# Optimization experiments

Hardware: AMD Instinct MI355X
Metric: run time of the kernel (lower is better)

The kernel has to match this reference:

```python
import jax, jax.numpy as jnp
import numpy as np

B, N, D, H = 4, 2048, 256, 8
d = D // H          # 32 per-head dim
EPS = 1e-5
SCALE = 1.0 / float(np.sqrt(d))


def setup_inputs() -> dict:
    key = jax.random.key(0)
    ks = jax.random.split(key, 6)
    s = 0.02
    x = jax.random.normal(ks[0], (B, N, D), jnp.float32)
    # RoPE frequencies: theta_j = 10000^(-2j/d), angle = pos * theta
    inv_freq = 1.0 / (10000.0 ** (jnp.arange(0, d, 2, dtype=jnp.float32) / d))  # (d/2,)
    ang = jnp.arange(N, dtype=jnp.float32)[:, None] * inv_freq[None, :]          # (N, d/2)
    return {
        "x": x,
        "freqs_cos": jnp.cos(ang),
        "freqs_sin": jnp.sin(ang),
        "w_qkv": jax.random.normal(ks[1], (D, 3 * D), jnp.float32) * s,
        "b_qkv": jnp.zeros((3 * D,), jnp.float32),
        "w_proj": jax.random.normal(ks[2], (D, D), jnp.float32) * s,
        "b_proj": jnp.zeros((D,), jnp.float32),
        "ln1_g": jnp.ones((D,), jnp.float32),
        "ln1_b": jnp.zeros((D,), jnp.float32),
        "ln2_g": jnp.ones((D,), jnp.float32),
        "ln2_b": jnp.zeros((D,), jnp.float32),
        "w1": jax.random.normal(ks[3], (D, 2 * D), jnp.float32) * s,
        "b1": jnp.zeros((2 * D,), jnp.float32),
        "w2": jax.random.normal(ks[4], (2 * D, D), jnp.float32) * s,
        "b2": jnp.zeros((D,), jnp.float32),
    }


def _layer_norm(x, g, b):
    mu = jnp.mean(x, axis=-1, keepdims=True)
    var = jnp.mean(jnp.square(x - mu), axis=-1, keepdims=True)
    return (x - mu) * jax.lax.rsqrt(var + EPS) * g + b


def _rope(t, cos, sin):
    # t: (B,H,N,d); interleaved (even,odd) pairs viewed as complex, multiplied by e^{i*ang}
    tr = t.reshape(B, H, N, d // 2, 2)
    te, to = tr[..., 0], tr[..., 1]
    c = cos[None, None, :, :]
    s = sin[None, None, :, :]
    oe = te * c - to * s
    oo = te * s + to * c
    return jnp.stack([oe, oo], axis=-1).reshape(B, H, N, d)


def reference(x, freqs_cos, freqs_sin, w_qkv, b_qkv, w_proj, b_proj,
              ln1_g, ln1_b, ln2_g, ln2_b, w1, b1, w2, b2):
    # Pre-LN MHSA with RoPE (dropout = identity at eval)
    h = _layer_norm(x, ln1_g, ln1_b)
    qkv = (h @ w_qkv + b_qkv).reshape(B, N, 3, H, d).transpose(0, 2, 3, 1, 4)  # (B,3,H,N,d)
    q, k, v = qkv[:, 0], qkv[:, 1], qkv[:, 2]
    q = _rope(q, freqs_cos, freqs_sin)
    k = _rope(k, freqs_cos, freqs_sin)
    attn = jax.nn.softmax(jnp.einsum('bhnd,bhmd->bhnm', q, k) * SCALE, axis=-1)
    out = jnp.einsum('bhnm,bhmd->bhnd', attn, v).transpose(0, 2, 1, 3).reshape(B, N, D)
    x = x + (out @ w_proj + b_proj)
    h = _layer_norm(x, ln2_g, ln2_b)
    ffn = jax.nn.relu(h @ w1 + b1) @ w2 + b2
    return x + ffn
```

## Files before the change

kernel.cpp:

```cpp
#include <hip/hip_runtime.h>
#include <hip/hip_bf16.h>
#include <math.h>

#define Bsz 4
#define Nseq 2048
#define Dm 256
#define Hh 8
#define Hd 32
#define EPS_ 1e-5f
#define SCALE_ 0.17677669529663687f
#define QSC_ (0.17677669529663687f * 1.4426950408889634f)

typedef __attribute__((ext_vector_type(8))) short short8;
typedef __attribute__((ext_vector_type(4))) short short4v;
typedef __attribute__((ext_vector_type(4))) float f32x4;
typedef __attribute__((ext_vector_type(16))) float f32x16;

__device__ __forceinline__ void gload16(const void* g, void* l) {
    __builtin_amdgcn_global_load_lds(
        (const __attribute__((address_space(1))) void*)g,
        (__attribute__((address_space(3))) void*)l, 16, 0, 0);
}

__device__ __forceinline__ short bf16s(float f) {
    __hip_bfloat16 h = __float2bfloat16(f);
    return *(short*)&h;
}

union FU { float f; unsigned u; };

__device__ __forceinline__ int pk2bf(float a, float b) {
    FU ua, ub; ua.f = a; ub.f = b;
    return (int)__builtin_amdgcn_perm(ub.u, ua.u, 0x07060302u);
}

union I4S8 { int i[4]; short8 s; };

__global__ __launch_bounds__(256) void prep_kernel(
    const float* __restrict__ x, const float* __restrict__ g1,
    const float* __restrict__ b1v, __hip_bfloat16* __restrict__ hout,
    const float* __restrict__ s0, const float* __restrict__ s1,
    const float* __restrict__ s2, const float* __restrict__ s3,
    __hip_bfloat16* __restrict__ d0, __hip_bfloat16* __restrict__ d1,
    __hip_bfloat16* __restrict__ d2, __hip_bfloat16* __restrict__ d3) {
    __shared__ float t[32][33];
    if (blockIdx.x < 2048) {
        int row  = blockIdx.x * 4 + (threadIdx.x >> 6);
        int lane = threadIdx.x & 63;
        const float* xr = x + (size_t)row * Dm;
        float4 v = *(const float4*)(xr + lane * 4);
        float s  = v.x + v.y + v.z + v.w;
        float ss = v.x * v.x + v.y * v.y + v.z * v.z + v.w * v.w;
        #pragma unroll
        for (int off = 32; off; off >>= 1) {
            s  += __shfl_xor(s, off);
            ss += __shfl_xor(ss, off);
        }
        float mu  = s * (1.0f / Dm);
        float var = ss * (1.0f / Dm) - mu * mu;
        float rs  = rsqrtf(var + EPS_);
        float4 gv = *(const float4*)(g1 + lane * 4);
        float4 bv = *(const float4*)(b1v + lane * 4);
        short4v o4 = { bf16s((v.x - mu) * rs * gv.x + bv.x),
                       bf16s((v.y - mu) * rs * gv.y + bv.y),
                       bf16s((v.z - mu) * rs * gv.z + bv.z),
                       bf16s((v.w - mu) * rs * gv.w + bv.w) };
        *(short4v*)(hout + (size_t)row * Dm + lane * 4) = o4;
        return;
    }
    int bid = blockIdx.x - 2048;
    const float* src; __hip_bfloat16* dst; int K, N, tb;
    if (bid < 192)      { src = s0; dst = d0; K = 256; N = 768; tb = bid; }
    else if (bid < 256) { src = s1; dst = d1; K = 256; N = 256; tb = bid - 192; }
    else if (bid < 384) { src = s2; dst = d2; K = 256; N = 512; tb = bid - 256; }
    else                { src = s3; dst = d3; K = 512; N = 256; tb = bid - 384; }
    int tn = N >> 5;
    int k0 = (tb / tn) * 32, n0 = (tb % tn) * 32;
    int c = threadIdx.x & 31, r0 = threadIdx.x >> 5;
    #pragma unroll
    for (int i = 0; i < 4; i++) {
        int r = r0 + i * 8;
        t[r][c] = src[(size_t)(k0 + r) * N + n0 + c];
    }
    __syncthreads();
    #pragma unroll
    for (int i = 0; i < 4; i++) {
        int n = r0 + i * 8;
        dst[(size_t)(n0 + n) * K + k0 + c] = __float2bfloat16(t[c][n]);
    }
}

__global__ __launch_bounds__(256) void ln_kernel(const float* __restrict__ x,
                                                 const float* __restrict__ g,
                                                 const float* __restrict__ b,
                                                 __hip_bfloat16* __restrict__ out) {
    int row  = blockIdx.x * 4 + (threadIdx.x >> 6);
    int lane = threadIdx.x & 63;
    const float* xr = x + (size_t)row * Dm;
    float4 v = *(const float4*)(xr + lane * 4);
    float s  = v.x + v.y + v.z + v.w;
    float ss = v.x * v.x + v.y * v.y + v.z * v.z + v.w * v.w;
    #pragma unroll
    for (int off = 32; off; off >>= 1) {
        s  += __shfl_xor(s, off);
        ss += __shfl_xor(ss, off);
    }
    float mu  = s * (1.0f / Dm);
    float var = ss * (1.0f / Dm) - mu * mu;
    float rs  = rsqrtf(var + EPS_);
    float4 gv = *(const float4*)(g + lane * 4);
    float4 bv = *(const float4*)(b + lane * 4);
    short4v o4 = { bf16s((v.x - mu) * rs * gv.x + bv.x),
                   bf16s((v.y - mu) * rs * gv.y + bv.y),
                   bf16s((v.z - mu) * rs * gv.z + bv.z),
                   bf16s((v.w - mu) * rs * gv.w + bv.w) };
    *(short4v*)(out + (size_t)row * Dm + lane * 4) = o4;
}

template <int EPI>
__global__ __launch_bounds__(256) void mfma_gemm(const __hip_bfloat16* __restrict__ A,
                                                 const __hip_bfloat16* __restrict__ Wt,
                                                 const float* __restrict__ bias,
                                                 const float* __restrict__ res,
                                                 float* __restrict__ Cf,
                                                 __hip_bfloat16* __restrict__ Cb,
                                                 int M, int Nn, int K) {
    __shared__ __align__(16) __hip_bfloat16 As[2][64 * 64];
    __shared__ __align__(16) __hip_bfloat16 Bs[2][64 * 64];
    const int tid = threadIdx.x, w = tid >> 6, lane = tid & 63;
    const int lm = lane & 15, lq = lane >> 4;
    const int bm = blockIdx.y * 64, bn = blockIdx.x * 64;
    f32x4 acc[4];
    #pragma unroll
    for (int j = 0; j < 4; j++) acc[j] = (f32x4){0.f, 0.f, 0.f, 0.f};

    const int sr = tid >> 3, ssl = tid & 7;
    const int sgk = (ssl ^ (sr & 7)) * 8;
    const int sr2 = 32 + sr;
    const int sgk2 = (ssl ^ (sr2 & 7)) * 8;

    gload16(A + (size_t)(bm + sr) * K + sgk, &As[0][w * 512]);
    gload16(A + (size_t)(bm + sr2) * K + sgk2, &As[0][2048 + w * 512]);
    gload16(Wt + (size_t)(bn + sr) * K + sgk, &Bs[0][w * 512]);
    gload16(Wt + (size_t)(bn + sr2) * K + sgk2, &Bs[0][2048 + w * 512]);

    const int arow = w * 16 + lm;
    const int ar7 = arow & 7, cr7base = lm & 7;
    for (int t = 0; t < K / 64; t++) {
        const int buf = t & 1;
        __syncthreads();
        if (t + 1 < K / 64) {
            int k0 = (t + 1) * 64;
            gload16(A + (size_t)(bm + sr) * K + k0 + sgk, &As[buf ^ 1][w * 512]);
            gload16(A + (size_t)(bm + sr2) * K + k0 + sgk2, &As[buf ^ 1][2048 + w * 512]);
            gload16(Wt + (size_t)(bn + sr) * K + k0 + sgk, &Bs[buf ^ 1][w * 512]);
            gload16(Wt + (size_t)(bn + sr2) * K + k0 + sgk2, &Bs[buf ^ 1][2048 + w * 512]);
        }
        #pragma unroll
        for (int ks = 0; ks < 2; ks++) {
            short8 a = *(const short8*)&As[buf][arow * 64 + (((ks * 4 + lq) ^ ar7) * 8)];
            #pragma unroll
            for (int nf = 0; nf < 4; nf++) {
                int cc = nf * 16 + lm;
                short8 bfr = *(const short8*)&Bs[buf][cc * 64 + (((ks * 4 + lq) ^ (cc & 7)) * 8)];
                acc[nf] = __builtin_amdgcn_mfma_f32_16x16x32_bf16(a, bfr, acc[nf], 0, 0, 0);
            }
        }
    }
    #pragma unroll
    for (int nf = 0; nf < 4; nf++) {
        int cg = bn + nf * 16 + lm;
        float bi = bias[cg];
        #pragma unroll
        for (int r = 0; r < 4; r++) {
            int rg = bm + w * 16 + lq * 4 + r;
            float v = acc[nf][r] + bi;
            if (EPI == 1) {
                v = fmaxf(v, 0.f);
                Cb[(size_t)rg * Nn + cg] = __float2bfloat16(v);
            } else {
                v += res[(size_t)rg * Nn + cg];
                Cf[(size_t)rg * Nn + cg] = v;
            }
        }
    }
}

__global__ __launch_bounds__(256) void qkv_mfma(const __hip_bfloat16* __restrict__ A,
                                                const __hip_bfloat16* __restrict__ Wt,
                                                const float* __restrict__ bias,
                                                const float* __restrict__ fcos,
                                                const float* __restrict__ fsin,
                                                __hip_bfloat16* __restrict__ qout,
                                                __hip_bfloat16* __restrict__ kout,
                                                __hip_bfloat16* __restrict__ vt) {
    const int K = 256;
    __shared__ __align__(16) __hip_bfloat16 As[2][64 * 64];
    __shared__ __align__(16) __hip_bfloat16 Bs[2][64 * 64];
    const int tid = threadIdx.x, w = tid >> 6, lane = tid & 63;
    const int lm = lane & 15, lq = lane >> 4;
    const int bm = blockIdx.y * 64, bn = blockIdx.x * 64;
    f32x4 acc[4];
    #pragma unroll
    for (int j = 0; j < 4; j++) acc[j] = (f32x4){0.f, 0.f, 0.f, 0.f};

    const int sr = tid >> 3, ssl = tid & 7;
    const int sgk = (ssl ^ (sr & 7)) * 8;
    const int sr2 = 32 + sr;
    const int sgk2 = (ssl ^ (sr2 & 7)) * 8;

    gload16(A + (size_t)(bm + sr) * K + sgk, &As[0][w * 512]);
    gload16(A + (size_t)(bm + sr2) * K + sgk2, &As[0][2048 + w * 512]);
    gload16(Wt + (size_t)(bn + sr) * K + sgk, &Bs[0][w * 512]);
    gload16(Wt + (size_t)(bn + sr2) * K + sgk2, &Bs[0][2048 + w * 512]);

    const int arow = w * 16 + lm;
    const int ar7 = arow & 7;
    for (int t = 0; t < K / 64; t++) {
        const int buf = t & 1;
        __syncthreads();
        if (t + 1 < K / 64) {
            int k0 = (t + 1) * 64;
            gload16(A + (size_t)(bm + sr) * K + k0 + sgk, &As[buf ^ 1][w * 512]);
            gload16(A + (size_t)(bm + sr2) * K + k0 + sgk2, &As[buf ^ 1][2048 + w * 512]);
            gload16(Wt + (size_t)(bn + sr) * K + k0 + sgk, &Bs[buf ^ 1][w * 512]);
            gload16(Wt + (size_t)(bn + sr2) * K + k0 + sgk2, &Bs[buf ^ 1][2048 + w * 512]);
        }
        #pragma unroll
        for (int ks = 0; ks < 2; ks++) {
            short8 a = *(const short8*)&As[buf][arow * 64 + (((ks * 4 + lq) ^ ar7) * 8)];
            #pragma unroll
            for (int nf = 0; nf < 4; nf++) {
                int cc = nf * 16 + lm;
                short8 bfr = *(const short8*)&Bs[buf][cc * 64 + (((ks * 4 + lq) ^ (cc & 7)) * 8)];
                acc[nf] = __builtin_amdgcn_mfma_f32_16x16x32_bf16(a, bfr, acc[nf], 0, 0, 0);
            }
        }
    }
    const int seg = bn >> 8;
    #pragma unroll
    for (int nf = 0; nf < 4; nf++) {
        int cg = bn + nf * 16 + lm;
        int hh = (cg & 255) >> 5;
        int dd = (nf & 1) * 16 + lm;
        int i0 = dd >> 1;
        float bi = bias[cg];
        #pragma unroll
        for (int r = 0; r < 4; r++) {
            int rg = bm + w * 16 + lq * 4 + r;
            int bb = rg >> 11, n = rg & (Nseq - 1);
            float v = acc[nf][r] + bi;
            if (seg == 2) {
                vt[(((size_t)(bb * Hh + hh)) * Hd + dd) * Nseq + n] = __float2bfloat16(v);
            } else {
                float vp = __shfl_xor(v, 1);
                float cs = fcos[n * 16 + i0], sn = fsin[n * 16 + i0];
                float outv = (dd & 1) ? (vp * sn + v * cs) : (v * cs - vp * sn);
                if (seg == 0) outv *= QSC_;
                __hip_bfloat16* dst = (seg == 0) ? qout : kout;
                dst[(((size_t)(bb * Hh + hh)) * Nseq + n) * Hd + dd] = __float2bfloat16(outv);
            }
        }
    }
}

__global__ __launch_bounds__(256) void attn_mfma(const __hip_bfloat16* __restrict__ q,
                                                 const __hip_bfloat16* __restrict__ k,
                                                 const __hip_bfloat16* __restrict__ vt,
                                                 __hip_bfloat16* __restrict__ att) {
    __shared__ __align__(16) char smem[4096 + 16384 + 16384 + 512];
    __hip_bfloat16* Qs  = (__hip_bfloat16*)smem;
    __hip_bfloat16* KsB = (__hip_bfloat16*)(smem + 4096);
    __hip_bfloat16* VsB = (__hip_bfloat16*)(smem + 20480);
    float* RedO = (float*)(smem + 4096);
    float* RedS = (float*)(smem + 4096 + 8192);
    float* smS  = (float*)(smem + 4096 + 8192 + 256);

    const int tid = threadIdx.x, w = tid >> 6, lane = tid & 63;
    const int l31 = lane & 31, hi = lane >> 5;
    const int wq = w >> 1, wk = w & 1;
    const int bh = blockIdx.y, qbase = blockIdx.x * 64;
    const __hip_bfloat16* qp = q + ((size_t)bh * Nseq + qbase) * Hd;
    const __hip_bfloat16* kp = k + (size_t)bh * Nseq * Hd;
    const __hip_bfloat16* vp = vt + (size_t)bh * Hd * Nseq;
    const int r8 = tid >> 3, s8 = tid & 7;

    {
        int r = tid >> 2, sl = tid & 3;
        gload16(qp + r * 32 + ((sl ^ (r & 3)) * 8), Qs + w * 512);
    }
    #pragma unroll
    for (int par = 0; par < 2; par++) {
        gload16(kp + (par * 64 + 2 * r8 + (s8 >> 2)) * 32 + (((s8 & 3) ^ (r8 & 3)) * 8),
                KsB + par * 2048 + w * 512);
        gload16(vp + (size_t)r8 * Nseq + par * 64 + ((s8 ^ (r8 & 7)) * 8),
                VsB + par * 2048 + w * 512);
    }
    __syncthreads();

    const int qrow = wq * 32 + l31;
    short8 qf0 = *(const short8*)&Qs[qrow * 32 + ((hi ^ (l31 & 3)) * 8)];
    short8 qf1 = *(const short8*)&Qs[qrow * 32 + (((2 + hi) ^ (l31 & 3)) * 8)];

    f32x16 O;
    #pragma unroll
    for (int i = 0; i < 16; i++) O[i] = 0.f;
    float sm = 0.f;

    for (int t = 0; t < 16; t++) {
        const int buf = t & 1;
        if (t + 1 < 16) {
            const int kb2 = (t + 1) * 128;
            #pragma unroll
            for (int par = 0; par < 2; par++) {
                gload16(kp + (kb2 + par * 64 + 2 * r8 + (s8 >> 2)) * 32 + (((s8 & 3) ^ (r8 & 3)) * 8),
                        KsB + ((buf ^ 1) * 2 + par) * 2048 + w * 512);
                gload16(vp + (size_t)r8 * Nseq + kb2 + par * 64 + ((s8 ^ (r8 & 7)) * 8),
                        VsB + ((buf ^ 1) * 2 + par) * 2048 + w * 512);
            }
        }
        const __hip_bfloat16* Kc = KsB + (buf * 2 + wk) * 2048;
        const __hip_bfloat16* Vc = VsB + (buf * 2 + wk) * 2048;
        f32x16 St0, St1;
        #pragma unroll
        for (int i = 0; i < 16; i++) { St0[i] = 0.f; St1[i] = 0.f; }
        {
            int pr = l31 >> 1, elb = pr * 64 + (l31 & 1) * 32;
            short8 kf0 = *(const short8*)&Kc[elb + ((hi ^ (pr & 3)) * 8)];
            short8 kf1 = *(const short8*)&Kc[elb + (((2 + hi) ^ (pr & 3)) * 8)];
            St0 = __builtin_amdgcn_mfma_f32_32x32x16_bf16(kf0, qf0, St0, 0, 0, 0);
            St0 = __builtin_amdgcn_mfma_f32_32x32x16_bf16(kf1, qf1, St0, 0, 0, 0);
        }
        {
            int pr = 16 + (l31 >> 1), elb = pr * 64 + (l31 & 1) * 32;
            short8 kf0 = *(const short8*)&Kc[elb + ((hi ^ (pr & 3)) * 8)];
            short8 kf1 = *(const short8*)&Kc[elb + (((2 + hi) ^ (pr & 3)) * 8)];
            St1 = __builtin_amdgcn_mfma_f32_32x32x16_bf16(kf0, qf0, St1, 0, 0, 0);
            St1 = __builtin_amdgcn_mfma_f32_32x32x16_bf16(kf1, qf1, St1, 0, 0, 0);
        }
        int pk0[8], pk1[8];
        #pragma unroll
        for (int p = 0; p < 8; p++) {
            float a = __builtin_amdgcn_exp2f(St0[2 * p]);
            float b = __builtin_amdgcn_exp2f(St0[2 * p + 1]);
            sm += a + b;
            pk0[p] = pk2bf(a, b);
        }
        #pragma unroll
        for (int p = 0; p < 8; p++) {
            float a = __builtin_amdgcn_exp2f(St1[2 * p]);
            float b = __builtin_amdgcn_exp2f(St1[2 * p + 1]);
            sm += a + b;
            pk1[p] = pk2bf(a, b);
        }
        #pragma unroll
        for (int tt = 0; tt < 4; tt++) {
            const int* PK = (tt >> 1) ? pk1 : pk0;
            const int base = 4 * (tt & 1);
            int keep0 = hi ? PK[base + 2] : PK[base + 0];
            int keep1 = hi ? PK[base + 3] : PK[base + 1];
            int send0 = hi ? PK[base + 0] : PK[base + 2];
            int send1 = hi ? PK[base + 1] : PK[base + 3];
            int x0 = __shfl_xor(send0, 32);
            int x1 = __shfl_xor(send1, 32);
            I4S8 u;
            u.i[0] = hi ? x0 : keep0;
            u.i[1] = hi ? x1 : keep1;
            u.i[2] = hi ? keep0 : x0;
            u.i[3] = hi ? keep1 : x1;
            short8 vf = *(const short8*)&Vc[l31 * 64 + (((2 * tt + hi) ^ (l31 & 7)) * 8)];
            O = __builtin_amdgcn_mfma_f32_32x32x16_bf16(u.s, vf, O, 0, 0, 0);
        }
        __syncthreads();
    }
    sm += __shfl_xor(sm, 32);
    if (wk == 1) {
        #pragma unroll
        for (int j = 0; j < 16; j++) RedO[(wq * 16 + j) * 64 + lane] = O[j];
        if (hi == 0) RedS[wq * 32 + l31] = sm;
    }
    __syncthreads();
    if (wk == 0) {
        #pragma unroll
        for (int j = 0; j < 16; j++) O[j] += RedO[(wq * 16 + j) * 64 + lane];
        sm += RedS[wq * 32 + l31];
        if (hi == 0) smS[wq * 32 + l31] = sm;
    }
    __syncthreads();
    if (wk == 0) {
        const int bb = bh >> 3, hh = bh & 7;
        #pragma unroll
        for (int m = 0; m < 4; m++) {
            float4 sv = *(const float4*)&smS[wq * 32 + 8 * m + 4 * hi];
            #pragma unroll
            for (int i = 0; i < 4; i++) {
                int n = qbase + wq * 32 + 8 * m + 4 * hi + i;
                att[((size_t)(bb * Nseq + n)) * Dm + hh * Hd + l31] =
                    __float2bfloat16(O[4 * m + i] * (1.0f / sv[i]));
            }
        }
    }
}

extern "C" void kernel_launch(void* const* d_in, const int* in_sizes, int n_in,
                              void* d_out, int out_size, void* d_ws, size_t ws_size,
                              hipStream_t stream) {
    const float* x      = (const float*)d_in[0];
    const float* fcos   = (const float*)d_in[1];
    const float* fsin   = (const float*)d_in[2];
    const float* w_qkv  = (const float*)d_in[3];
    const float* b_qkv  = (const float*)d_in[4];
    const float* w_proj = (const float*)d_in[5];
    const float* b_proj = (const float*)d_in[6];
    const float* ln1_g  = (const float*)d_in[7];
    const float* ln1_b  = (const float*)d_in[8];
    const float* ln2_g  = (const float*)d_in[9];
    const float* ln2_b  = (const float*)d_in[10];
    const float* w1     = (const float*)d_in[11];
    const float* b1     = (const float*)d_in[12];
    const float* w2     = (const float*)d_in[13];
    const float* b2     = (const float*)d_in[14];
    float* out = (float*)d_out;
    char* base = (char*)d_ws;
    const size_t MB = (size_t)1 << 20;

    __hip_bfloat16* h   = (__hip_bfloat16*)(base);
    __hip_bfloat16* qb  = (__hip_bfloat16*)(base + 4 * MB);
    __hip_bfloat16* kbf = (__hip_bfloat16*)(base + 8 * MB);
    __hip_bfloat16* vtb = (__hip_bfloat16*)(base + 12 * MB);
    __hip_bfloat16* att = (__hip_bfloat16*)(base + 16 * MB);
    float*          x2f = (float*)(base + 20 * MB);
    __hip_bfloat16* h2  = (__hip_bfloat16*)(base);
    __hip_bfloat16* ffn = (__hip_bfloat16*)(base + 28 * MB);
    __hip_bfloat16* wqT = (__hip_bfloat16*)(base + 40 * MB);
    __hip_bfloat16* wpT = (__hip_bfloat16*)(base + 40 * MB + 393216);
    __hip_bfloat16* w1T = (__hip_bfloat16*)(base + 40 * MB + 524288);
    __hip_bfloat16* w2T = (__hip_bfloat16*)(base + 40 * MB + 786432);

    const int rows = Bsz * Nseq;

    prep_kernel<<<2560, 256, 0, stream>>>(x, ln1_g, ln1_b, h,
                                          w_qkv, w_proj, w1, w2, wqT, wpT, w1T, w2T);
    qkv_mfma<<<dim3(12, 128), 256, 0, stream>>>(h, wqT, b_qkv, fcos, fsin, qb, kbf, vtb);
    attn_mfma<<<dim3(Nseq / 64, Bsz * Hh), 256, 0, stream>>>(qb, kbf, vtb, att);
    mfma_gemm<2><<<dim3(4, 128), 256, 0, stream>>>(att, wpT, b_proj, x, x2f, nullptr,
                                                   rows, 256, 256);
    ln_kernel<<<rows / 4, 256, 0, stream>>>(x2f, ln2_g, ln2_b, h2);
    mfma_gemm<1><<<dim3(8, 128), 256, 0, stream>>>(h2, w1T, b1, nullptr, nullptr, ffn,
                                                   rows, 512, 256);
    mfma_gemm<2><<<dim3(4, 128), 256, 0, stream>>>(ffn, w2T, b2, x2f, out, nullptr,
                                                   rows, 256, 512);
}
```

Before: 174.2 us.

## Fuse out-projection, LayerNorm2 and FFN into one per-row-tile tail kernel

```diff
diff --git a/kernel.cpp b/kernel.cpp
--- a/kernel.cpp
+++ b/kernel.cpp
@@ -87,102 +87,6 @@
     for (int i = 0; i < 4; i++) {
         int n = r0 + i * 8;
         dst[(size_t)(n0 + n) * K + k0 + c] = __float2bfloat16(t[c][n]);
-    }
-}
-
-__global__ __launch_bounds__(256) void ln_kernel(const float* __restrict__ x,
-                                                 const float* __restrict__ g,
-                                                 const float* __restrict__ b,
-                                                 __hip_bfloat16* __restrict__ out) {
-    int row  = blockIdx.x * 4 + (threadIdx.x >> 6);
-    int lane = threadIdx.x & 63;
-    const float* xr = x + (size_t)row * Dm;
-    float4 v = *(const float4*)(xr + lane * 4);
-    float s  = v.x + v.y + v.z + v.w;
-    float ss = v.x * v.x + v.y * v.y + v.z * v.z + v.w * v.w;
-    #pragma unroll
-    for (int off = 32; off; off >>= 1) {
-        s  += __shfl_xor(s, off);
-        ss += __shfl_xor(ss, off);
-    }
-    float mu  = s * (1.0f / Dm);
-    float var = ss * (1.0f / Dm) - mu * mu;
-    float rs  = rsqrtf(var + EPS_);
-    float4 gv = *(const float4*)(g + lane * 4);
-    float4 bv = *(const float4*)(b + lane * 4);
-    short4v o4 = { bf16s((v.x - mu) * rs * gv.x + bv.x),
-                   bf16s((v.y - mu) * rs * gv.y + bv.y),
-                   bf16s((v.z - mu) * rs * gv.z + bv.z),
-                   bf16s((v.w - mu) * rs * gv.w + bv.w) };
-    *(short4v*)(out + (size_t)row * Dm + lane * 4) = o4;
-}
-
-template <int EPI>
-__global__ __launch_bounds__(256) void mfma_gemm(const __hip_bfloat16* __restrict__ A,
-                                                 const __hip_bfloat16* __restrict__ Wt,
-                                                 const float* __restrict__ bias,
-                                                 const float* __restrict__ res,
-                                                 float* __restrict__ Cf,
-                                                 __hip_bfloat16* __restrict__ Cb,
-                                                 int M, int Nn, int K) {
-    __shared__ __align__(16) __hip_bfloat16 As[2][64 * 64];
-    __shared__ __align__(16) __hip_bfloat16 Bs[2][64 * 64];
-    const int tid = threadIdx.x, w = tid >> 6, lane = tid & 63;
-    const int lm = lane & 15, lq = lane >> 4;
-    const int bm = blockIdx.y * 64, bn = blockIdx.x * 64;
-    f32x4 acc[4];
-    #pragma unroll
-    for (int j = 0; j < 4; j++) acc[j] = (f32x4){0.f, 0.f, 0.f, 0.f};
-
-    const int sr = tid >> 3, ssl = tid & 7;
-    const int sgk = (ssl ^ (sr & 7)) * 8;
-    const int sr2 = 32 + sr;
-    const int sgk2 = (ssl ^ (sr2 & 7)) * 8;
-
-    gload16(A + (size_t)(bm + sr) * K + sgk, &As[0][w * 512]);
-    gload16(A + (size_t)(bm + sr2) * K + sgk2, &As[0][2048 + w * 512]);
-    gload16(Wt + (size_t)(bn + sr) * K + sgk, &Bs[0][w * 512]);
-    gload16(Wt + (size_t)(bn + sr2) * K + sgk2, &Bs[0][2048 + w * 512]);
-
-    const int arow = w * 16 + lm;
-    const int ar7 = arow & 7, cr7base = lm & 7;
-    for (int t = 0; t < K / 64; t++) {
-        const int buf = t & 1;
-        __syncthreads();
-        if (t + 1 < K / 64) {
-            int k0 = (t + 1) * 64;
-            gload16(A + (size_t)(bm + sr) * K + k0 + sgk, &As[buf ^ 1][w * 512]);
-            gload16(A + (size_t)(bm + sr2) * K + k0 + sgk2, &As[buf ^ 1][2048 + w * 512]);
-            gload16(Wt + (size_t)(bn + sr) * K + k0 + sgk, &Bs[buf ^ 1][w * 512]);
-            gload16(Wt + (size_t)(bn + sr2) * K + k0 + sgk2, &Bs[buf ^ 1][2048 + w * 512]);
-        }
-        #pragma unroll
-        for (int ks = 0; ks < 2; ks++) {
-            short8 a = *(const short8*)&As[buf][arow * 64 + (((ks * 4 + lq) ^ ar7) * 8)];
-            #pragma unroll
-            for (int nf = 0; nf < 4; nf++) {
-                int cc = nf * 16 + lm;
-                short8 bfr = *(const short8*)&Bs[buf][cc * 64 + (((ks * 4 + lq) ^ (cc & 7)) * 8)];
-                acc[nf] = __builtin_amdgcn_mfma_f32_16x16x32_bf16(a, bfr, acc[nf], 0, 0, 0);
-            }
-        }
-    }
-    #pragma unroll
-    for (int nf = 0; nf < 4; nf++) {
-        int cg = bn + nf * 16 + lm;
-        float bi = bias[cg];
-        #pragma unroll
-        for (int r = 0; r < 4; r++) {
-            int rg = bm + w * 16 + lq * 4 + r;
-            float v = acc[nf][r] + bi;
-            if (EPI == 1) {
-                v = fmaxf(v, 0.f);
-                Cb[(size_t)rg * Nn + cg] = __float2bfloat16(v);
-            } else {
-                v += res[(size_t)rg * Nn + cg];
-                Cf[(size_t)rg * Nn + cg] = v;
-            }
-        }
     }
 }
 
@@ -399,6 +303,256 @@
                     __float2bfloat16(O[4 * m + i] * (1.0f / sv[i]));
             }
         }
+    }
+}
+
+__global__ __launch_bounds__(256, 1) void tail_fused(
+    const __hip_bfloat16* __restrict__ att, const __hip_bfloat16* __restrict__ wpT,
+    const float* __restrict__ b_proj, const float* __restrict__ x,
+    const float* __restrict__ g2, const float* __restrict__ bv2,
+    const __hip_bfloat16* __restrict__ w1T, const float* __restrict__ b1,
+    const __hip_bfloat16* __restrict__ w2T, const float* __restrict__ b2,
+    float* __restrict__ out) {
+    __shared__ __align__(16) __hip_bfloat16 WS[2][4][4096];
+    __shared__ __align__(16) __hip_bfloat16 AH[8192];
+    __shared__ __align__(16) __hip_bfloat16 PS[16384];
+    __shared__ float red[4][32][2];
+    __shared__ float muS[32], rsS[32];
+
+    const int tid = threadIdx.x, w = tid >> 6, lane = tid & 63;
+    const int lm = lane & 15, lq = lane >> 4;
+    const int R0 = blockIdx.x * 32;
+    const int c0 = w * 64;
+    const int c0f = w * 128;
+
+    {
+        const int srow = tid >> 3, ssl = tid & 7;
+        #pragma unroll
+        for (int kt = 0; kt < 4; kt++)
+            gload16(att + (size_t)(R0 + srow) * 256 + kt * 64 + ((ssl ^ (srow & 7)) * 8),
+                    AH + kt * 2048 + w * 512);
+    }
+    #pragma unroll
+    for (int ri = 0; ri < 8; ri++) {
+        int r = ri * 8 + (lane >> 3), sl = lane & 7;
+        gload16(wpT + (size_t)(c0 + r) * 256 + ((sl ^ (r & 7)) * 8), &WS[0][w][ri * 512]);
+    }
+    __syncthreads();
+
+    short8 aF[2][4][2];
+    #pragma unroll
+    for (int mf = 0; mf < 2; mf++) {
+        int r = mf * 16 + lm;
+        #pragma unroll
+        for (int kt = 0; kt < 4; kt++)
+            #pragma unroll
+            for (int ks = 0; ks < 2; ks++)
+                aF[mf][kt][ks] = *(const short8*)&AH[kt * 2048 + r * 64 +
+                                                    (((ks * 4 + lq) ^ (lm & 7)) * 8)];
+    }
+    float xr[2][4][4];
+    #pragma unroll
+    for (int mf = 0; mf < 2; mf++)
+        #pragma unroll
+        for (int r = 0; r < 4; r++) {
+            int row = R0 + mf * 16 + lq * 4 + r;
+            #pragma unroll
+            for (int nf = 0; nf < 4; nf++)
+                xr[mf][nf][r] = x[(size_t)row * 256 + c0 + nf * 16 + lm];
+        }
+
+    f32x4 acc[2][4];
+    #pragma unroll
+    for (int i = 0; i < 2; i++)
+        #pragma unroll
+        for (int j = 0; j < 4; j++) acc[i][j] = (f32x4){0.f, 0.f, 0.f, 0.f};
+    for (int kt = 0; kt < 4; kt++) {
+        const int buf = kt & 1;
+        if (kt) __syncthreads();
+        if (kt + 1 < 4) {
+            #pragma unroll
+            for (int ri = 0; ri < 8; ri++) {
+                int r = ri * 8 + (lane >> 3), sl = lane & 7;
+                gload16(wpT + (size_t)(c0 + r) * 256 + (kt + 1) * 64 + ((sl ^ (r & 7)) * 8),
+                        &WS[buf ^ 1][w][ri * 512]);
+            }
+        }
+        #pragma unroll
+        for (int ks = 0; ks < 2; ks++)
+            #pragma unroll
+            for (int nf = 0; nf < 4; nf++) {
+                int cc = nf * 16 + lm;
+                short8 bfr = *(const short8*)&WS[buf][w][cc * 64 + (((ks * 4 + lq) ^ (lm & 7)) * 8)];
+                #pragma unroll
+                for (int mf = 0; mf < 2; mf++)
+                    acc[mf][nf] = __builtin_amdgcn_mfma_f32_16x16x32_bf16(
+                        aF[mf][kt][ks], bfr, acc[mf][nf], 0, 0, 0);
+            }
+    }
+    #pragma unroll
+    for (int nf = 0; nf < 4; nf++) {
+        float bp = b_proj[c0 + nf * 16 + lm];
+        #pragma unroll
+        for (int mf = 0; mf < 2; mf++)
+            #pragma unroll
+            for (int r = 0; r < 4; r++) xr[mf][nf][r] += acc[mf][nf][r] + bp;
+    }
+
+    #pragma unroll
+    for (int mf = 0; mf < 2; mf++)
+        #pragma unroll
+        for (int r = 0; r < 4; r++) {
+            float s = 0.f, ss = 0.f;
+            #pragma unroll
+            for (int nf = 0; nf < 4; nf++) {
+                float v = xr[mf][nf][r];
+                s += v; ss += v * v;
+            }
+            #pragma unroll
+            for (int off = 1; off <= 8; off <<= 1) {
+                s  += __shfl_xor(s, off);
+                ss += __shfl_xor(ss, off);
+            }
+            if (lm == 0) {
+                int row = mf * 16 + lq * 4 + r;
+                red[w][row][0] = s;
+                red[w][row][1] = ss;
+            }
+        }
+    #pragma unroll
+    for (int ri = 0; ri < 8; ri++) {
+        int r = ri * 16 + (lane >> 2), sl = lane & 3;
+        gload16(w1T + (size_t)(c0f + r) * 256 + ((sl ^ (r & 3)) * 8), &WS[0][w][ri * 512]);
+    }
+    __syncthreads();
+    if (tid < 32) {
+        float s = red[0][tid][0] + red[1][tid][0] + red[2][tid][0] + red[3][tid][0];
+        float ss = red[0][tid][1] + red[1][tid][1] + red[2][tid][1] + red[3][tid][1];
+        float mu = s * (1.0f / 256.0f);
+        muS[tid] = mu;
+        rsS[tid] = rsqrtf(ss * (1.0f / 256.0f) - mu * mu + EPS_);
+    }
+    __syncthreads();
+    #pragma unroll
+    for (int mf = 0; mf < 2; mf++)
+        #pragma unroll
+        for (int r = 0; r < 4; r++) {
+            int row = mf * 16 + lq * 4 + r;
+            float mu = muS[row], rs = rsS[row];
+            int rw7 = row & 7;
+            #pragma unroll
+            for (int nf = 0; nf < 4; nf++) {
+                int c = c0 + nf * 16 + lm;
+                float h = (xr[mf][nf][r] - mu) * rs * g2[c] + bv2[c];
+                int slc = nf * 2 + (lm >> 3);
+                AH[w * 2048 + row * 64 + ((slc ^ rw7) * 8) + (lm & 7)] = __float2bfloat16(h);
+            }
+        }
+    __syncthreads();
+
+    f32x4 acc2[2][8];
+    #pragma unroll
+    for (int i = 0; i < 2; i++)
+        #pragma unroll
+        for (int j = 0; j < 8; j++) acc2[i][j] = (f32x4){0.f, 0.f, 0.f, 0.f};
+    for (int kt = 0; kt < 8; kt++) {
+        const int buf = kt & 1;
+        if (kt) __syncthreads();
+        if (kt + 1 < 8) {
+            #pragma unroll
+            for (int ri = 0; ri < 8; ri++) {
+                int r = ri * 16 + (lane >> 2), sl = lane & 3;
+                gload16(w1T + (size_t)(c0f + r) * 256 + (kt + 1) * 32 + ((sl ^ (r & 3)) * 8),
+                        &WS[buf ^ 1][w][ri * 512]);
+            }
+        }
+        short8 aA[2];
+        #pragma unroll
+        for (int mf = 0; mf < 2; mf++) {
+            int r = mf * 16 + lm;
+            aA[mf] = *(const short8*)&AH[(kt >> 1) * 2048 + r * 64 +
+                                         ((((kt & 1) * 4 + lq) ^ (lm & 7)) * 8)];
+        }
+        #pragma unroll
+        for (int nf = 0; nf < 8; nf++) {
+            int cc = nf * 16 + lm;
+            short8 bfr = *(const short8*)&WS[buf][w][cc * 32 + ((lq ^ (lm & 3)) * 8)];
+            #pragma unroll
+            for (int mf = 0; mf < 2; mf++)
+                acc2[mf][nf] = __builtin_amdgcn_mfma_f32_16x16x32_bf16(
+                    aA[mf], bfr, acc2[mf][nf], 0, 0, 0);
+        }
+    }
+    #pragma unroll
+    for (int ri = 0; ri < 8; ri++) {
+        int r = ri * 8 + (lane >> 3), sl = lane & 7;
+        gload16(w2T + (size_t)(c0 + r) * 512 + ((sl ^ (r & 7)) * 8), &WS[0][w][ri * 512]);
+    }
+    #pragma unroll
+    for (int nf = 0; nf < 8; nf++) {
+        int c = c0f + nf * 16 + lm;
+        float bb1 = b1[c];
+        int kt8 = w * 2 + (nf >> 2);
+        int slc = (nf & 3) * 2 + (lm >> 3);
+        #pragma unroll
+        for (int mf = 0; mf < 2; mf++)
+            #pragma unroll
+            for (int r = 0; r < 4; r++) {
+                int row = mf * 16 + lq * 4 + r;
+                float p = fmaxf(acc2[mf][nf][r] + bb1, 0.f);
+                PS[kt8 * 2048 + row * 64 + ((slc ^ (row & 7)) * 8) + (lm & 7)] =
+                    __float2bfloat16(p);
+            }
+    }
+    __syncthreads();
+
+    f32x4 acc3[2][4];
+    #pragma unroll
+    for (int i = 0; i < 2; i++)
+        #pragma unroll
+        for (int j = 0; j < 4; j++) acc3[i][j] = (f32x4){0.f, 0.f, 0.f, 0.f};
+    for (int kt = 0; kt < 8; kt++) {
+        const int buf = kt & 1;
+        if (kt) __syncthreads();
+        if (kt + 1 < 8) {
+            #pragma unroll
+            for (int ri = 0; ri < 8; ri++) {
+                int r = ri * 8 + (lane >> 3), sl = lane & 7;
+                gload16(w2T + (size_t)(c0 + r) * 512 + (kt + 1) * 64 + ((sl ^ (r & 7)) * 8),
+                        &WS[buf ^ 1][w][ri * 512]);
+            }
+        }
+        #pragma unroll
+        for (int ks = 0; ks < 2; ks++) {
+            short8 aP[2];
+            #pragma unroll
+            for (int mf = 0; mf < 2; mf++) {
+                int r = mf * 16 + lm;
+                aP[mf] = *(const short8*)&PS[kt * 2048 + r * 64 +
+                                             (((ks * 4 + lq) ^ (lm & 7)) * 8)];
+            }
+            #pragma unroll
+            for (int nf = 0; nf < 4; nf++) {
+                int cc = nf * 16 + lm;
+                short8 bfr = *(const short8*)&WS[buf][w][cc * 64 + (((ks * 4 + lq) ^ (lm & 7)) * 8)];
+                #pragma unroll
+                for (int mf = 0; mf < 2; mf++)
+                    acc3[mf][nf] = __builtin_amdgcn_mfma_f32_16x16x32_bf16(
+                        aP[mf], bfr, acc3[mf][nf], 0, 0, 0);
+            }
+        }
+    }
+    #pragma unroll
+    for (int nf = 0; nf < 4; nf++) {
+        int c = c0 + nf * 16 + lm;
+        float bb2 = b2[c];
+        #pragma unroll
+        for (int mf = 0; mf < 2; mf++)
+            #pragma unroll
+            for (int r = 0; r < 4; r++) {
+                int row = R0 + mf * 16 + lq * 4 + r;
+                out[(size_t)row * 256 + c] = acc3[mf][nf][r] + bb2 + xr[mf][nf][r];
+            }
     }
 }
 
@@ -429,25 +583,15 @@
     __hip_bfloat16* kbf = (__hip_bfloat16*)(base + 8 * MB);
     __hip_bfloat16* vtb = (__hip_bfloat16*)(base + 12 * MB);
     __hip_bfloat16* att = (__hip_bfloat16*)(base + 16 * MB);
-    float*          x2f = (float*)(base + 20 * MB);
-    __hip_bfloat16* h2  = (__hip_bfloat16*)(base);
-    __hip_bfloat16* ffn = (__hip_bfloat16*)(base + 28 * MB);
-    __hip_bfloat16* wqT = (__hip_bfloat16*)(base + 40 * MB);
-    __hip_bfloat16* wpT = (__hip_bfloat16*)(base + 40 * MB + 393216);
-    __hip_bfloat16* w1T = (__hip_bfloat16*)(base + 40 * MB + 524288);
-    __hip_bfloat16* w2T = (__hip_bfloat16*)(base + 40 * MB + 786432);
-
-    const int rows = Bsz * Nseq;
+    __hip_bfloat16* wqT = (__hip_bfloat16*)(base + 20 * MB);
+    __hip_bfloat16* wpT = (__hip_bfloat16*)(base + 20 * MB + 393216);
+    __hip_bfloat16* w1T = (__hip_bfloat16*)(base + 20 * MB + 524288);
+    __hip_bfloat16* w2T = (__hip_bfloat16*)(base + 20 * MB + 786432);
 
     prep_kernel<<<2560, 256, 0, stream>>>(x, ln1_g, ln1_b, h,
                                           w_qkv, w_proj, w1, w2, wqT, wpT, w1T, w2T);
     qkv_mfma<<<dim3(12, 128), 256, 0, stream>>>(h, wqT, b_qkv, fcos, fsin, qb, kbf, vtb);
     attn_mfma<<<dim3(Nseq / 64, Bsz * Hh), 256, 0, stream>>>(qb, kbf, vtb, att);
-    mfma_gemm<2><<<dim3(4, 128), 256, 0, stream>>>(att, wpT, b_proj, x, x2f, nullptr,
-                                                   rows, 256, 256);
-    ln_kernel<<<rows / 4, 256, 0, stream>>>(x2f, ln2_g, ln2_b, h2);
-    mfma_gemm<1><<<dim3(8, 128), 256, 0, stream>>>(h2, w1T, b1, nullptr, nullptr, ffn,
-                                                   rows, 512, 256);
-    mfma_gemm<2><<<dim3(4, 128), 256, 0, stream>>>(ffn, w2T, b2, x2f, out, nullptr,
-                                                   rows, 256, 512);
-}
+    tail_fused<<<256, 256, 0, stream>>>(att, wpT, b_proj, x, ln2_g, ln2_b,
+                                        w1T, b1, w2T, b2, out);
+}
```

After: 172.5 us. No clear change (-1.0%).
